# Kernel optimization log

Measured on AMD Instinct MI355X. Metric: run time of the kernel, lower is better.

Reference implementation:

```python
import jax, jax.numpy as jnp
import numpy as np
import math

N_EMBD = 1024
BATCH = 8
T = 2048
INIT_DECAY = 0.95


def setup_inputs() -> dict:
    key = jax.random.key(0)
    k1, k2 = jax.random.split(key)
    raw_init = math.log(INIT_DECAY / (1.0 - INIT_DECAY))
    x = jax.random.normal(k1, (BATCH, T, N_EMBD), dtype=jnp.float32)
    raw_a = jnp.full((N_EMBD,), raw_init, dtype=jnp.float32)
    B = jax.random.normal(k2, (N_EMBD, N_EMBD), dtype=jnp.float32) * 0.01
    h0 = jnp.zeros((BATCH, N_EMBD), dtype=jnp.float32)
    return {"x": x, "raw_a": raw_a, "B": B, "h0": h0}


def reference(x, raw_a, B, h0):
    # a: [H] diagonal decay in (0,1)
    a = jax.nn.sigmoid(raw_a)
    # Precompute the dense projection for all timesteps at once: u[b,t,h] = x[b,t,:] @ B.T
    u = jnp.einsum('btc,hc->bth', x, B)
    # Diagonal linear recurrence h_t = a * h_{t-1} + u_t via lax.scan over time.
    u_t_first = jnp.swapaxes(u, 0, 1)  # [T, B, H]

    def step(h, u_t):
        h = h * a + u_t
        return h, h

    _, ys = jax.lax.scan(step, h0, u_t_first)  # ys: [T, B, H]
    return jnp.swapaxes(ys, 0, 1)  # [B, T, H]
```

## Files before the change

kernel.cpp:

```cpp
#include <hip/hip_runtime.h>
#include <hip/hip_bf16.h>

using bf16 = __hip_bfloat16;
typedef __attribute__((ext_vector_type(8))) short frag8;
typedef __attribute__((ext_vector_type(4))) float f32x4;

constexpr int   H_   = 1024;
constexpr int   B_   = 8;
constexpr int   T_   = 2048;
constexpr int   K_   = H_;
constexpr int   N_   = H_;
constexpr long  M_   = (long)B_ * T_;
constexpr int   SEG  = 64;
constexpr int   TSEG = T_ / SEG;
constexpr int   NCH  = B_ * H_;
constexpr int   NVC  = NCH / 4;

__device__ __forceinline__ unsigned short f2bf(float f) {
  bf16 b = __float2bfloat16(f);
  return *reinterpret_cast<unsigned short*>(&b);
}

__device__ __forceinline__ float4 fma4(float4 h, float4 a, float4 v) {
  float4 r;
  r.x = fmaf(h.x, a.x, v.x);
  r.y = fmaf(h.y, a.y, v.y);
  r.z = fmaf(h.z, a.z, v.z);
  r.w = fmaf(h.w, a.w, v.w);
  return r;
}

__global__ __launch_bounds__(256) void k_convert(const float* __restrict__ x,
                                                 const float* __restrict__ Bm,
                                                 const float* __restrict__ raw,
                                                 unsigned short* __restrict__ xb,
                                                 unsigned short* __restrict__ Bb,
                                                 float* __restrict__ a_sig) {
  const long NX4 = (M_ * K_) / 4;
  const long NB4 = ((long)N_ * K_) / 4;
  long t = (long)blockIdx.x * 256 + threadIdx.x;
  const float* src; unsigned short* dst;
  if (t < NX4) { src = x; dst = xb; }
  else if (t < NX4 + NB4) { t -= NX4; src = Bm; dst = Bb; }
  else {
    long q = t - NX4 - NB4;
    if (q >= H_ / 4) return;
    float4 v = *reinterpret_cast<const float4*>(raw + q * 4);
    float4 o;
    o.x = 1.0f / (1.0f + expf(-v.x));
    o.y = 1.0f / (1.0f + expf(-v.y));
    o.z = 1.0f / (1.0f + expf(-v.z));
    o.w = 1.0f / (1.0f + expf(-v.w));
    *reinterpret_cast<float4*>(a_sig + q * 4) = o;
    return;
  }
  long i = t * 4;
  float4 v = *reinterpret_cast<const float4*>(src + i);
  short4 o;
  o.x = (short)f2bf(v.x);
  o.y = (short)f2bf(v.y);
  o.z = (short)f2bf(v.z);
  o.w = (short)f2bf(v.w);
  *reinterpret_cast<short4*>(dst + i) = o;
}

#define MEMBAR asm volatile("" ::: "memory")
#define BARR do { MEMBAR; __builtin_amdgcn_s_barrier(); MEMBAR; } while (0)
#define VMW(n) asm volatile("s_waitcnt vmcnt(" #n ")" ::: "memory")
#define GLDS(SRC, DST) __builtin_amdgcn_global_load_lds( \
    (const __attribute__((address_space(1))) void*)(SRC), \
    (__attribute__((address_space(3))) void*)(DST), 16, 0, 0)

__global__ __launch_bounds__(512, 2) void k_gemm(const unsigned short* __restrict__ A,
                                                 const unsigned short* __restrict__ Bb,
                                                 float* __restrict__ C) {
  __shared__ __align__(16) unsigned short lA[32768];
  __shared__ __align__(16) unsigned short lB[32768];
  const int tid  = threadIdx.x;
  const int wid  = tid >> 6, lane = tid & 63;
  const int wr   = wid >> 2, wc = wid & 3;
  const int quad = lane >> 4, l16 = lane & 15;
  const int sx   = l16 & 7;
  const int bh   = wc >> 1, br = (wc & 1) * 64;
  const int bid  = blockIdx.x;
  const int wgid = (bid & 7) * 32 + (bid >> 3);
  const long m0 = (long)(wgid >> 2) * 256;
  const long n0 = (long)(wgid & 3) * 256;
  const int sgran = (tid & 7) ^ ((tid >> 3) & 7);
  const unsigned short* gA = A  + (m0 + (tid >> 3)) * K_ + sgran * 8;
  const unsigned short* gB = Bb + (n0 + (tid >> 3)) * K_ + sgran * 8;
  unsigned short* sAw = lA + wid * 512;
  unsigned short* sBw = lB + wid * 512;

#define STG_A(d, hf, t) do { \
    GLDS(gA + ((hf) * 128) * K_ + (t) * 64,      sAw + (d) * 16384 + (hf) * 8192); \
    GLDS(gA + ((hf) * 128 + 64) * K_ + (t) * 64, sAw + (d) * 16384 + (hf) * 8192 + 4096); } while (0)
#define STG_B(d, hf, t) do { \
    GLDS(gB + ((hf) * 128) * K_ + (t) * 64,      sBw + (d) * 16384 + (hf) * 8192); \
    GLDS(gB + ((hf) * 128 + 64) * K_ + (t) * 64, sBw + (d) * 16384 + (hf) * 8192 + 4096); } while (0)

  f32x4 acc[8][4];
  #pragma unroll
  for (int i = 0; i < 8; i++)
    #pragma unroll
    for (int j = 0; j < 4; j++) acc[i][j] = f32x4{0.f, 0.f, 0.f, 0.f};

  frag8 aR[4][2];
  frag8 bR[2][2][2];

#define RD_A(d, ih) do { _Pragma("unroll") \
    for (int ii = 0; ii < 4; ii++) { \
      const unsigned short* rp = lA + (d) * 16384 + wr * 8192 + (((ih) * 4 + ii) * 16 + l16) * 64; \
      aR[ii][0] = *(const frag8*)(rp + (quad ^ sx) * 8); \
      aR[ii][1] = *(const frag8*)(rp + ((quad + 4) ^ sx) * 8); } } while (0)
#define RD_B(d, jh) do { _Pragma("unroll") \
    for (int jj = 0; jj < 2; jj++) { \
      const unsigned short* rp = lB + (d) * 16384 + bh * 8192 + (br + ((jh) * 2 + jj) * 16 + l16) * 64; \
      bR[jh][jj][0] = *(const frag8*)(rp + (quad ^ sx) * 8); \
      bR[jh][jj][1] = *(const frag8*)(rp + ((quad + 4) ^ sx) * 8); } } while (0)
#define MMQ(ih, jh) do { __builtin_amdgcn_s_setprio(1); _Pragma("unroll") \
    for (int ii = 0; ii < 4; ii++) { _Pragma("unroll") \
      for (int jj = 0; jj < 2; jj++) { \
        acc[(ih)*4+ii][(jh)*2+jj] = __builtin_amdgcn_mfma_f32_16x16x32_bf16(aR[ii][0], bR[jh][jj][0], acc[(ih)*4+ii][(jh)*2+jj], 0, 0, 0); \
        acc[(ih)*4+ii][(jh)*2+jj] = __builtin_amdgcn_mfma_f32_16x16x32_bf16(aR[ii][1], bR[jh][jj][1], acc[(ih)*4+ii][(jh)*2+jj], 0, 0, 0); } } \
    __builtin_amdgcn_s_setprio(0); } while (0)

  STG_A(0, 0, 0); STG_A(0, 1, 0); STG_B(0, 0, 0); STG_B(0, 1, 0); STG_A(1, 0, 1);
  VMW(2); BARR;

  for (int it = 0; it < 7; ++it) {
    const int to = 2 * it + 1, te2 = 2 * it + 2, to2 = 2 * it + 3;
    RD_A(0, 0); RD_B(0, 0); STG_A(1, 1, to);          BARR; MMQ(0, 0);
    RD_B(0, 1);             STG_B(1, 0, to);          BARR; MMQ(0, 1);
    RD_A(0, 1);             STG_B(1, 1, to);          BARR; MMQ(1, 1);
                            STG_A(0, 0, te2); VMW(2); BARR; MMQ(1, 0);
    RD_A(1, 0); RD_B(1, 0); STG_A(0, 1, te2);         BARR; MMQ(0, 0);
    RD_B(1, 1);             STG_B(0, 0, te2);         BARR; MMQ(0, 1);
    RD_A(1, 1);             STG_B(0, 1, te2);         BARR; MMQ(1, 1);
                            STG_A(1, 0, to2); VMW(2); BARR; MMQ(1, 0);
  }
  RD_A(0, 0); RD_B(0, 0); STG_A(1, 1, 15);         BARR; MMQ(0, 0);
  RD_B(0, 1);             STG_B(1, 0, 15);         BARR; MMQ(0, 1);
  RD_A(0, 1);             STG_B(1, 1, 15);         BARR; MMQ(1, 1);
                                           VMW(0); BARR; MMQ(1, 0);
  RD_A(1, 0); RD_B(1, 0);                          BARR; MMQ(0, 0);
  RD_B(1, 1);                                      BARR; MMQ(0, 1);
  RD_A(1, 1);                                      BARR; MMQ(1, 1);
  MMQ(1, 0);

  #pragma unroll
  for (int i = 0; i < 8; i++)
    #pragma unroll
    for (int j = 0; j < 4; j++) {
      const long r0 = m0 + wr * 128 + i * 16 + quad * 4;
      const long c0 = n0 + wc * 64 + j * 16 + l16;
      #pragma unroll
      for (int r = 0; r < 4; r++)
        C[(r0 + r) * N_ + c0] = acc[i][j][r];
    }
}

__global__ __launch_bounds__(256) void k_seg_ends(const float* __restrict__ u,
                                                  const float* __restrict__ a_sig,
                                                  float* __restrict__ E) {
  int g = blockIdx.x * 256 + threadIdx.x;
  int vc = g & (NVC - 1);
  int s  = g >> 11;
  int b  = vc >> 8;
  int h4 = (vc & 255) * 4;
  float4 a = *reinterpret_cast<const float4*>(a_sig + h4);
  const float* base = u + (long)b * T_ * H_ + (long)s * TSEG * H_ + h4;
  float4 e = {0.f, 0.f, 0.f, 0.f};
  #pragma unroll
  for (int t0 = 0; t0 < TSEG; t0 += 8) {
    float4 v[8];
    #pragma unroll
    for (int j = 0; j < 8; j++)
      v[j] = *reinterpret_cast<const float4*>(base + (long)(t0 + j) * H_);
    #pragma unroll
    for (int j = 0; j < 8; j++)
      e = fma4(e, a, v[j]);
  }
  *reinterpret_cast<float4*>(E + (long)g * 4) = e;
}

__global__ __launch_bounds__(256) void k_scan(float* __restrict__ u,
                                              const float* __restrict__ E,
                                              const float* __restrict__ h0,
                                              const float* __restrict__ a_sig) {
  int g = blockIdx.x * 256 + threadIdx.x;
  int vc = g & (NVC - 1);
  int s  = g >> 11;
  int b  = vc >> 8;
  int h4 = (vc & 255) * 4;
  float4 a = *reinterpret_cast<const float4*>(a_sig + h4);
  float4 aL = a;
  #pragma unroll
  for (int i = 0; i < 5; i++) { aL.x *= aL.x; aL.y *= aL.y; aL.z *= aL.z; aL.w *= aL.w; }
  float4 hs = *reinterpret_cast<const float4*>(h0 + (long)vc * 4);
  int j = 0;
  for (; j + 8 <= s; j += 8) {
    float4 e[8];
    #pragma unroll
    for (int q = 0; q < 8; q++)
      e[q] = *reinterpret_cast<const float4*>(E + (long)(j + q) * NCH + (long)vc * 4);
    #pragma unroll
    for (int q = 0; q < 8; q++)
      hs = fma4(hs, aL, e[q]);
  }
  for (; j < s; ++j) {
    float4 e = *reinterpret_cast<const float4*>(E + (long)j * NCH + (long)vc * 4);
    hs = fma4(hs, aL, e);
  }

  float* base = u + (long)b * T_ * H_ + (long)s * TSEG * H_ + h4;

  float4 v0[8], v1[8];
  #pragma unroll
  for (int jj = 0; jj < 8; jj++)
    v0[jj] = *reinterpret_cast<const float4*>(base + (long)jj * H_);

  #pragma unroll
  for (int t0 = 0; t0 < TSEG; t0 += 8) {
    const bool odd = (t0 >> 3) & 1;
    float4* cur = odd ? v1 : v0;
    float4* nxt = odd ? v0 : v1;
    if (t0 + 8 < TSEG) {
      #pragma unroll
      for (int jj = 0; jj < 8; jj++)
        nxt[jj] = *reinterpret_cast<const float4*>(base + (long)(t0 + 8 + jj) * H_);
    }
    #pragma unroll
    for (int jj = 0; jj < 8; jj++) {
      hs = fma4(hs, a, cur[jj]);
      cur[jj] = hs;
    }
    #pragma unroll
    for (int jj = 0; jj < 8; jj++)
      *reinterpret_cast<float4*>(base + (long)(t0 + jj) * H_) = cur[jj];
  }
}

extern "C" void kernel_launch(void* const* d_in, const int* in_sizes, int n_in,
                              void* d_out, int out_size, void* d_ws, size_t ws_size,
                              hipStream_t stream) {
  const float* x    = (const float*)d_in[0];
  const float* rawa = (const float*)d_in[1];
  const float* Bm   = (const float*)d_in[2];
  const float* h0   = (const float*)d_in[3];
  float* u = (float*)d_out;

  char* w = (char*)d_ws;
  unsigned short* xb = (unsigned short*)w;
  unsigned short* Bb = (unsigned short*)(w + 33554432);
  float* a_sig = (float*)(w + 33554432 + 2097152);
  float* E     = (float*)(w + 33554432 + 2097152 + 4096);

  hipLaunchKernelGGL(k_convert, dim3(17409), dim3(256), 0, stream, x, Bm, rawa, xb, Bb, a_sig);
  hipLaunchKernelGGL(k_gemm, dim3(256), dim3(512), 0, stream, xb, Bb, u);
  hipLaunchKernelGGL(k_seg_ends, dim3(NVC * SEG / 256), dim3(256), 0, stream, u, a_sig, E);
  hipLaunchKernelGGL(k_scan, dim3(NVC * SEG / 256), dim3(256), 0, stream, u, E, h0, a_sig);
}
```

Baseline: 181.7 us.

## Fuse segment-end recurrence reduction into GEMM epilogue from register accumulators

Removes the separate k_seg_ends kernel, which re-read the whole 64MB u tensor to compute per-segment decayed sums. The GEMM epilogue now computes those sums straight from the accumulator registers: a Horner evaluation over each quad's 4 rows, scaling by powers of a^4, and a cross-quad shuffle reduction, with one write to E per 32-row segment. This saves a full pass over u plus a kernel launch, at the cost of extra epilogue arithmetic and register pressure in the GEMM.

```diff
diff --git a/kernel.cpp b/kernel.cpp
--- a/kernel.cpp
+++ b/kernel.cpp
@@ -73,7 +73,9 @@
 
 __global__ __launch_bounds__(512, 2) void k_gemm(const unsigned short* __restrict__ A,
                                                  const unsigned short* __restrict__ Bb,
-                                                 float* __restrict__ C) {
+                                                 float* __restrict__ C,
+                                                 const float* __restrict__ a_sig,
+                                                 float* __restrict__ E) {
   __shared__ __align__(16) unsigned short lA[32768];
   __shared__ __align__(16) unsigned short lB[32768];
   const int tid  = threadIdx.x;
@@ -158,30 +160,35 @@
       for (int r = 0; r < 4; r++)
         C[(r0 + r) * N_ + c0] = acc[i][j][r];
     }
-}
-
-__global__ __launch_bounds__(256) void k_seg_ends(const float* __restrict__ u,
-                                                  const float* __restrict__ a_sig,
-                                                  float* __restrict__ E) {
-  int g = blockIdx.x * 256 + threadIdx.x;
-  int vc = g & (NVC - 1);
-  int s  = g >> 11;
-  int b  = vc >> 8;
-  int h4 = (vc & 255) * 4;
-  float4 a = *reinterpret_cast<const float4*>(a_sig + h4);
-  const float* base = u + (long)b * T_ * H_ + (long)s * TSEG * H_ + h4;
-  float4 e = {0.f, 0.f, 0.f, 0.f};
-  #pragma unroll
-  for (int t0 = 0; t0 < TSEG; t0 += 8) {
-    float4 v[8];
-    #pragma unroll
-    for (int j = 0; j < 8; j++)
-      v[j] = *reinterpret_cast<const float4*>(base + (long)(t0 + j) * H_);
-    #pragma unroll
-    for (int j = 0; j < 8; j++)
-      e = fma4(e, a, v[j]);
-  }
-  *reinterpret_cast<float4*>(E + (long)g * 4) = e;
+
+  {
+    const int bb = (int)(m0 >> 11);
+    const int sB = (int)((m0 & 2047) >> 5);
+    #pragma unroll
+    for (int j = 0; j < 4; j++) {
+      const int c0 = (int)(n0) + wc * 64 + j * 16 + l16;
+      const float a  = a_sig[c0];
+      const float a2 = a * a, a4 = a2 * a2;
+      float p4[8];
+      p4[0] = 1.f;
+      #pragma unroll
+      for (int k = 1; k < 8; k++) p4[k] = p4[k - 1] * a4;
+      #pragma unroll
+      for (int sp = 0; sp < 4; sp++) {
+        const f32x4 v = acc[sp * 2][j];
+        const f32x4 w = acc[sp * 2 + 1][j];
+        float p0 = ((v[0] * a + v[1]) * a + v[2]) * a + v[3];
+        float p1 = ((w[0] * a + w[1]) * a + w[2]) * a + w[3];
+        float e = p4[7 - quad] * p0 + p4[3 - quad] * p1;
+        e += __shfl_xor(e, 16, 64);
+        e += __shfl_xor(e, 32, 64);
+        if (quad == 0) {
+          const int sg = sB + wr * 4 + sp;
+          E[(long)sg * NCH + bb * H_ + c0] = e;
+        }
+      }
+    }
+  }
 }
 
 __global__ __launch_bounds__(256) void k_scan(float* __restrict__ u,
@@ -257,7 +264,6 @@
   float* E     = (float*)(w + 33554432 + 2097152 + 4096);
 
   hipLaunchKernelGGL(k_convert, dim3(17409), dim3(256), 0, stream, x, Bm, rawa, xb, Bb, a_sig);
-  hipLaunchKernelGGL(k_gemm, dim3(256), dim3(512), 0, stream, xb, Bb, u);
-  hipLaunchKernelGGL(k_seg_ends, dim3(NVC * SEG / 256), dim3(256), 0, stream, u, a_sig, E);
+  hipLaunchKernelGGL(k_gemm, dim3(256), dim3(512), 0, stream, xb, Bb, u, a_sig, E);
   hipLaunchKernelGGL(k_scan, dim3(NVC * SEG / 256), dim3(256), 0, stream, u, E, h0, a_sig);
 }
```

After: 172.3 us. 5.2% less time.
